# Kernel optimization log

Measured on AMD Instinct MI355X. Metric: run time of the kernel, lower is better.

Reference implementation:

```python
import jax, jax.numpy as jnp
import numpy as np

EMBED_DIM = 256
DEPTH = 4
N_EMBED = 8192
COMMIT_W = 0.25


def setup_inputs() -> dict:
    key = jax.random.key(0)
    kx, kc = jax.random.split(key)
    x = jax.random.normal(kx, (8, 1024, EMBED_DIM), dtype=jnp.float32)
    # stacked per-depth codebooks, last row is the padding row (unused by argmin path)
    codebooks = jax.random.normal(kc, (DEPTH, N_EMBED + 1, EMBED_DIM), dtype=jnp.float32) * 0.05
    return {"x": x, "codebooks": codebooks}


def _quantize_once(residual, cb):
    # residual: [..., D], cb: [K, D]
    D = cb.shape[-1]
    flat = residual.reshape(-1, D)                              # [N, D]
    dist = (jnp.sum(flat * flat, axis=1, keepdims=True)
            + jnp.sum(cb * cb, axis=1)[None, :]
            - 2.0 * (flat @ cb.T))                              # [N, K]
    idx = jnp.argmin(dist, axis=-1)                             # [N]
    quant = cb[idx].reshape(residual.shape)                     # gather
    return quant, idx.reshape(residual.shape[:-1])


def reference(x, codebooks):
    depth = codebooks.shape[0]
    residual = jax.lax.stop_gradient(x)
    agg = jnp.zeros_like(x)
    loss = jnp.float32(0.0)
    codes = []
    for d in range(depth):  # small fixed depth loop (structurally distinct codebooks)
        cb = jax.lax.stop_gradient(codebooks[d, :-1, :])        # drop padding row
        quant, idx = _quantize_once(residual, cb)
        residual = residual - quant
        agg = agg + quant                                       # partial-sum quant at depth d
        codes.append(idx)
        # commitment loss term: mse(x, partial_quant.detach())
        loss = loss + jnp.mean((x - jax.lax.stop_gradient(agg)) ** 2)
    commitment_loss = COMMIT_W * loss / depth
    # straight-through estimator
    out = x + jax.lax.stop_gradient(agg - x)
    code_idxs = jnp.stack(codes, axis=-1)                       # [..., depth]
    return out, commitment_loss, code_idxs
```

## Files before the change

kernel.cpp:

```cpp
#include <hip/hip_runtime.h>

#define NTOK   8192
#define DIM    256
#define NDEPTH 4
#define KROWS  8193
#define KARG   8192
#define NSLICE 8
#define FCAP   1024
#define EPSGAP 3e-3f

typedef __attribute__((ext_vector_type(8))) short short8v;
typedef __attribute__((ext_vector_type(4))) float float4v;

__device__ __forceinline__ unsigned short f2bf(float f) {
    unsigned int u = __float_as_uint(f);
    unsigned int r = (u + 0x7FFFu + ((u >> 16) & 1u)) >> 16;
    return (unsigned short)r;
}

__device__ __forceinline__ size_t fragIdx(int tile, int s, int lane, int e) {
    return ((((size_t)tile * 8 + s) * 64 + lane) * 8 + e);
}

__global__ void prep_tokens0(const float* __restrict__ x, unsigned short* __restrict__ rhB,
                             unsigned short* __restrict__ rlB, double* __restrict__ r64) {
    int t = blockIdx.x, i = threadIdx.x;
    float v = x[(size_t)t * DIM + i];
    r64[(size_t)t * DIM + i] = (double)v;
    unsigned short hb = f2bf(v);
    float hf = __uint_as_float(((unsigned int)hb) << 16);
    unsigned short lb = f2bf(v - hf);
    int T = t >> 4, n = t & 15;
    int s = i >> 5, kl = i & 31, g = kl >> 3, e = kl & 7;
    size_t idx = fragIdx(T, s, g * 16 + n, e);
    rhB[idx] = hb;
    rlB[idx] = lb;
}

__global__ void cnorm_kernel(const float* __restrict__ cbs, double* __restrict__ cnorm64,
                             float* __restrict__ cnorm32) {
    int d    = blockIdx.y;
    int row  = blockIdx.x * 4 + (threadIdx.x >> 6);
    int lane = threadIdx.x & 63;
    const float* c = cbs + ((size_t)d * KROWS + row) * DIM;
    float4 v = *(const float4*)(c + lane * 4);
    double s = (double)v.x * v.x + (double)v.y * v.y + (double)v.z * v.z + (double)v.w * v.w;
    #pragma unroll
    for (int o = 32; o > 0; o >>= 1) s += __shfl_down(s, o, 64);
    if (lane == 0) {
        cnorm64[(size_t)d * KARG + row] = s;
        cnorm32[(size_t)d * KARG + row] = (float)s;
    }
}

__global__ void prep_codes(const float* __restrict__ cbs, unsigned short* __restrict__ chA,
                           unsigned short* __restrict__ clA) {
    int bid = blockIdx.x;
    int d = bid >> 13, j = bid & 8191;
    int i = threadIdx.x;
    float v = cbs[((size_t)d * KROWS + j) * DIM + i];
    unsigned short hb = f2bf(v);
    float hf = __uint_as_float(((unsigned int)hb) << 16);
    unsigned short lb = f2bf(v - hf);
    int CT = j >> 4, m = j & 15;
    int s = i >> 5, kl = i & 31, g = kl >> 3, e = kl & 7;
    size_t base = (size_t)d * KARG * DIM;
    size_t idx = base + fragIdx(CT, s, g * 16 + m, e);
    chA[idx] = hb;
    clA[idx] = lb;
}

__global__ __launch_bounds__(512, 2) void argmin_mfma2(const unsigned short* __restrict__ chA_d,
                                                       const unsigned short* __restrict__ clA_d,
                                                       const unsigned short* __restrict__ rhB,
                                                       const unsigned short* __restrict__ rlB,
                                                       const float* __restrict__ cn32_d,
                                                       float* __restrict__ sM1, int* __restrict__ sJ1,
                                                       float* __restrict__ sM2) {
    __shared__ unsigned short lds[2][2][16384];
    const int tid  = threadIdx.x;
    const int wave = tid >> 6, lane = tid & 63;
    const int tg = blockIdx.x >> 3, slice = blockIdx.x & 7;
    const int g4 = lane >> 4, col = lane & 15;
    const float INF = __int_as_float(0x7f800000);

    const int T = tg * 8 + wave;
    short8v bh[8], bl[8];
    #pragma unroll
    for (int s = 0; s < 8; ++s) {
        bh[s] = *(const short8v*)(rhB + fragIdx(T, s, lane, 0));
        bl[s] = *(const short8v*)(rlB + fragIdx(T, s, lane, 0));
    }

    typedef const __attribute__((address_space(1))) unsigned int GUI;
    typedef __attribute__((address_space(3))) unsigned int LUI;
    auto stage = [&](int buf, int cg) {
        const unsigned short* gh = chA_d + ((size_t)(slice * 64 + cg * 4)) * 4096;
        const unsigned short* gl = clA_d + ((size_t)(slice * 64 + cg * 4)) * 4096;
        #pragma unroll
        for (int p = 0; p < 4; ++p) {
            int off = (p * 512 + tid) * 8;
            __builtin_amdgcn_global_load_lds((GUI*)(gh + off), (LUI*)(&lds[buf][0][off]), 16, 0, 0);
            __builtin_amdgcn_global_load_lds((GUI*)(gl + off), (LUI*)(&lds[buf][1][off]), 16, 0, 0);
        }
    };

    float M1 = INF, M2 = INF;
    int   J1 = 0;

    stage(0, 0);
    int buf = 0;
    for (int cg = 0; cg < 16; ++cg) {
        float4 cn[4];
        #pragma unroll
        for (int ct = 0; ct < 4; ++ct)
            cn[ct] = *(const float4*)(cn32_d + (slice * 64 + cg * 4 + ct) * 16 + g4 * 4);
        stage(buf ^ 1, cg + 1);
        asm volatile("s_waitcnt vmcnt(12)" ::: "memory");
        __builtin_amdgcn_s_barrier();

        float4v acc[4];
        #pragma unroll
        for (int ct = 0; ct < 4; ++ct) acc[ct] = (float4v){0.f, 0.f, 0.f, 0.f};
        #pragma unroll
        for (int s = 0; s < 8; ++s) {
            #pragma unroll
            for (int ct = 0; ct < 4; ++ct) {
                short8v ah = *(const short8v*)&lds[buf][0][((ct * 8 + s) * 64 + lane) * 8];
                short8v al = *(const short8v*)&lds[buf][1][((ct * 8 + s) * 64 + lane) * 8];
                acc[ct] = __builtin_amdgcn_mfma_f32_16x16x32_bf16(ah, bh[s], acc[ct], 0, 0, 0);
                acc[ct] = __builtin_amdgcn_mfma_f32_16x16x32_bf16(ah, bl[s], acc[ct], 0, 0, 0);
                acc[ct] = __builtin_amdgcn_mfma_f32_16x16x32_bf16(al, bh[s], acc[ct], 0, 0, 0);
            }
        }
        #pragma unroll
        for (int ct = 0; ct < 4; ++ct) {
            const int jb = (slice * 64 + cg * 4 + ct) * 16 + g4 * 4;
            float dv;
            dv = cn[ct].x - 2.0f * acc[ct][0];
            if (dv < M1) { M2 = M1; M1 = dv; J1 = jb + 0; } else if (dv < M2) M2 = dv;
            dv = cn[ct].y - 2.0f * acc[ct][1];
            if (dv < M1) { M2 = M1; M1 = dv; J1 = jb + 1; } else if (dv < M2) M2 = dv;
            dv = cn[ct].z - 2.0f * acc[ct][2];
            if (dv < M1) { M2 = M1; M1 = dv; J1 = jb + 2; } else if (dv < M2) M2 = dv;
            dv = cn[ct].w - 2.0f * acc[ct][3];
            if (dv < M1) { M2 = M1; M1 = dv; J1 = jb + 3; } else if (dv < M2) M2 = dv;
        }
        __builtin_amdgcn_s_barrier();
        buf ^= 1;
    }

    #pragma unroll
    for (int off = 16; off <= 32; off <<= 1) {
        float om1 = __shfl_xor(M1, off, 64);
        int   oj  = __shfl_xor(J1, off, 64);
        float om2 = __shfl_xor(M2, off, 64);
        if (om1 < M1 || (om1 == M1 && oj < J1)) {
            M2 = fminf(M1, om2); M1 = om1; J1 = oj;
        } else {
            M2 = fminf(M2, om1);
        }
    }
    if (g4 == 0) {
        int t = tg * 128 + wave * 16 + col;
        sM1[slice * NTOK + t] = M1;
        sJ1[slice * NTOK + t] = J1;
        sM2[slice * NTOK + t] = M2;
    }
}

__global__ void merge_flag8(const float* __restrict__ sM1, const int* __restrict__ sJ1,
                            const float* __restrict__ sM2, int* __restrict__ idxv,
                            int* __restrict__ flagList, int* __restrict__ flagCount) {
    int t = blockIdx.x * 256 + threadIdx.x;
    float m1 = sM1[t], m2 = sM2[t];
    int   j1 = sJ1[t];
    #pragma unroll
    for (int s = 1; s < NSLICE; ++s) {
        float a1 = sM1[s * NTOK + t], a2 = sM2[s * NTOK + t];
        int   aj = sJ1[s * NTOK + t];
        if (a1 < m1) { m2 = fminf(m1, a2); m1 = a1; j1 = aj; }
        else         { m2 = fminf(m2, a1); }
    }
    idxv[t] = j1;
    if (m2 - m1 <= EPSGAP) {
        int pos = atomicAdd(flagCount, 1);
        if (pos < FCAP) flagList[pos] = t;
    }
}

__global__ __launch_bounds__(256) void recheck_part(const double* __restrict__ rsrc,
                                                    const float* __restrict__ cb,
                                                    const double* __restrict__ cnorm,
                                                    const int* __restrict__ flagList,
                                                    const int* __restrict__ flagCount,
                                                    double* __restrict__ partD,
                                                    int* __restrict__ partJ) {
    const int slot = blockIdx.x >> 3;
    const int cnt  = min(*flagCount, FCAP);
    if (slot >= cnt) return;
    const int range = blockIdx.x & 7;
    const int tid   = threadIdx.x;
    const int tok   = flagList[slot];
    __shared__ double rs[DIM];
    __shared__ double sbest[256];
    __shared__ int    sbidx[256];
    rs[tid] = rsrc[(size_t)tok * DIM + tid];
    __syncthreads();

    double best = 1e300; int bestj = 0;
    for (int q = 0; q < 4; ++q) {
        const int j = range * 1024 + q * 256 + tid;
        const float* c = cb + (size_t)j * DIM;
        double acc = 0.0;
        #pragma unroll 1
        for (int i = 0; i < DIM; i += 4) {
            float4 cv = *(const float4*)(c + i);
            acc = fma((double)cv.w, rs[i + 3],
                  fma((double)cv.z, rs[i + 2],
                  fma((double)cv.y, rs[i + 1],
                  fma((double)cv.x, rs[i + 0], acc))));
        }
        double dist = cnorm[j] - 2.0 * acc;
        if (dist < best) { best = dist; bestj = j; }
    }
    sbest[tid] = best; sbidx[tid] = bestj;
    __syncthreads();
    for (int s = 128; s > 0; s >>= 1) {
        if (tid < s) {
            double ob = sbest[tid + s]; int oj = sbidx[tid + s];
            if (ob < sbest[tid] || (ob == sbest[tid] && oj < sbidx[tid])) {
                sbest[tid] = ob; sbidx[tid] = oj;
            }
        }
        __syncthreads();
    }
    if (tid == 0) { partD[slot * 8 + range] = sbest[0]; partJ[slot * 8 + range] = sbidx[0]; }
}

__global__ void recheck_merge(const int* __restrict__ flagList, const int* __restrict__ flagCount,
                              const double* __restrict__ partD, const int* __restrict__ partJ,
                              int* __restrict__ idxv) {
    int slot = blockIdx.x * 256 + threadIdx.x;
    int cnt  = min(*flagCount, FCAP);
    if (slot >= cnt) return;
    double best = partD[slot * 8]; int bestj = partJ[slot * 8];
    #pragma unroll
    for (int r = 1; r < 8; ++r) {
        double ob = partD[slot * 8 + r]; int oj = partJ[slot * 8 + r];
        if (ob < best) { best = ob; bestj = oj; }
    }
    idxv[flagList[slot]] = bestj;
}

__global__ void update_kernel(const float* __restrict__ x, const float* __restrict__ cb,
                              const int* __restrict__ idxv, double* __restrict__ resid,
                              float* __restrict__ out, double* __restrict__ lossSum,
                              float* __restrict__ codes_out, unsigned short* __restrict__ rhB,
                              unsigned short* __restrict__ rlB, int is_first) {
    const int t = blockIdx.x;
    const int i = threadIdx.x;
    const int idx = idxv[t];
    const size_t off = (size_t)t * DIM + i;
    float q = cb[(size_t)idx * DIM + i];
    double r_new = resid[off] - (double)q;
    resid[off] = r_new;
    float rv = (float)r_new;
    unsigned short hb = f2bf(rv);
    float hf = __uint_as_float(((unsigned int)hb) << 16);
    unsigned short lb = f2bf(rv - hf);
    {
        int T = t >> 4, n = t & 15;
        int s = i >> 5, kl = i & 31, g = kl >> 3, e = kl & 7;
        size_t fi = fragIdx(T, s, g * 16 + n, e);
        rhB[fi] = hb; rlB[fi] = lb;
    }
    float a_new = is_first ? q : (out[off] + q);
    out[off] = a_new;
    float diff = x[off] - a_new;
    double v = (double)diff * (double)diff;
    #pragma unroll
    for (int o = 32; o > 0; o >>= 1) v += __shfl_down(v, o, 64);
    __shared__ double wsum[4];
    int wid = i >> 6, lane = i & 63;
    if (lane == 0) wsum[wid] = v;
    __syncthreads();
    if (i == 0) {
        atomicAdd(lossSum, wsum[0] + wsum[1] + wsum[2] + wsum[3]);
        codes_out[(size_t)t * NDEPTH] = (float)idx;
    }
}

__global__ void final_kernel(float* __restrict__ out, const double* __restrict__ lossSum) {
    if (threadIdx.x == 0) {
        double s = (lossSum[0] + lossSum[1] + lossSum[2] + lossSum[3]) / (double)((size_t)NTOK * DIM);
        out[(size_t)NTOK * DIM] = (float)(0.25 * s / (double)NDEPTH);
    }
}

extern "C" void kernel_launch(void* const* d_in, const int* in_sizes, int n_in,
                              void* d_out, int out_size, void* d_ws, size_t ws_size,
                              hipStream_t stream) {
    const float* x   = (const float*)d_in[0];
    const float* cbs = (const float*)d_in[1];
    float* out = (float*)d_out;
    char* ws = (char*)d_ws;

    double*         resid64  = (double*)(ws);
    unsigned short* chA      = (unsigned short*)(ws + 16777216);
    unsigned short* clA      = (unsigned short*)(ws + 33554432);
    unsigned short* rhB      = (unsigned short*)(ws + 50331648);
    unsigned short* rlB      = (unsigned short*)(ws + 54525952);
    double*         cnorm64  = (double*)(ws + 58720256);
    float*          cnorm32  = (float*)(ws + 58982400);
    float*          sM1      = (float*)(ws + 59113472);
    int*            sJ1      = (int*)  (ws + 59375616);
    float*          sM2      = (float*)(ws + 59637760);
    int*            idxbuf   = (int*)  (ws + 59899904);
    int*            flagList = (int*)  (ws + 59932672);
    double*         partD    = (double*)(ws + 59936768);
    int*            partJ    = (int*)  (ws + 60002304);
    int*            flagCount= (int*)  (ws + 60035072);
    double*         lossSum  = (double*)(ws + 60035088);

    hipMemsetAsync(lossSum, 0, NDEPTH * sizeof(double), stream);
    prep_tokens0<<<NTOK, 256, 0, stream>>>(x, rhB, rlB, resid64);
    cnorm_kernel<<<dim3(KARG / 4, NDEPTH), 256, 0, stream>>>(cbs, cnorm64, cnorm32);
    prep_codes<<<NDEPTH * KARG, 256, 0, stream>>>(cbs, chA, clA);

    float* codes_base = out + (size_t)NTOK * DIM + 1;
    for (int d = 0; d < NDEPTH; ++d) {
        const float* cbd = cbs + (size_t)d * KROWS * DIM;
        hipMemsetAsync(flagCount, 0, sizeof(int), stream);
        argmin_mfma2<<<512, 512, 0, stream>>>(chA + (size_t)d * KARG * DIM,
                                              clA + (size_t)d * KARG * DIM,
                                              rhB, rlB, cnorm32 + (size_t)d * KARG,
                                              sM1, sJ1, sM2);
        merge_flag8<<<NTOK / 256, 256, 0, stream>>>(sM1, sJ1, sM2, idxbuf, flagList, flagCount);
        recheck_part<<<FCAP * 8, 256, 0, stream>>>(resid64, cbd, cnorm64 + (size_t)d * KARG,
                                                   flagList, flagCount, partD, partJ);
        recheck_merge<<<FCAP / 256, 256, 0, stream>>>(flagList, flagCount, partD, partJ, idxbuf);
        update_kernel<<<NTOK, 256, 0, stream>>>(x, cbd, idxbuf, resid64, out,
                                                lossSum + d, codes_base + d, rhB, rlB,
                                                d == 0 ? 1 : 0);
    }
    final_kernel<<<1, 64, 0, stream>>>(out, lossSum);
}
```

Measured before the change: 1.322 ms.

## Double token tiles per wave in argmin, fuse prep kernels and recheck merge

Each wave in the MFMA argmin kernel now processes two 16-token tiles instead of one, so every codebook fragment staged in LDS is reused across twice as many tokens and the grid is halved. The three preprocessing kernels are merged into one launch, with the code-norm reduction moved into the codebook-prep blocks. The recheck-merge kernel is folded into the update kernel through a per-token flag slot, and the per-depth memsets become one memset of per-depth counters. In exchange the argmin kernel holds more registers for B fragments and accumulators, and fewer blocks are launched.

Measured after the change: 1.217 ms. 7.9% less time.

```diff
diff --git a/kernel.cpp b/kernel.cpp
--- a/kernel.cpp
+++ b/kernel.cpp
@@ -22,55 +22,54 @@
     return ((((size_t)tile * 8 + s) * 64 + lane) * 8 + e);
 }
 
-__global__ void prep_tokens0(const float* __restrict__ x, unsigned short* __restrict__ rhB,
-                             unsigned short* __restrict__ rlB, double* __restrict__ r64) {
-    int t = blockIdx.x, i = threadIdx.x;
-    float v = x[(size_t)t * DIM + i];
-    r64[(size_t)t * DIM + i] = (double)v;
-    unsigned short hb = f2bf(v);
-    float hf = __uint_as_float(((unsigned int)hb) << 16);
-    unsigned short lb = f2bf(v - hf);
-    int T = t >> 4, n = t & 15;
-    int s = i >> 5, kl = i & 31, g = kl >> 3, e = kl & 7;
-    size_t idx = fragIdx(T, s, g * 16 + n, e);
-    rhB[idx] = hb;
-    rlB[idx] = lb;
-}
-
-__global__ void cnorm_kernel(const float* __restrict__ cbs, double* __restrict__ cnorm64,
-                             float* __restrict__ cnorm32) {
-    int d    = blockIdx.y;
-    int row  = blockIdx.x * 4 + (threadIdx.x >> 6);
-    int lane = threadIdx.x & 63;
-    const float* c = cbs + ((size_t)d * KROWS + row) * DIM;
-    float4 v = *(const float4*)(c + lane * 4);
-    double s = (double)v.x * v.x + (double)v.y * v.y + (double)v.z * v.z + (double)v.w * v.w;
-    #pragma unroll
-    for (int o = 32; o > 0; o >>= 1) s += __shfl_down(s, o, 64);
-    if (lane == 0) {
-        cnorm64[(size_t)d * KARG + row] = s;
-        cnorm32[(size_t)d * KARG + row] = (float)s;
-    }
-}
-
-__global__ void prep_codes(const float* __restrict__ cbs, unsigned short* __restrict__ chA,
-                           unsigned short* __restrict__ clA) {
-    int bid = blockIdx.x;
-    int d = bid >> 13, j = bid & 8191;
-    int i = threadIdx.x;
-    float v = cbs[((size_t)d * KROWS + j) * DIM + i];
-    unsigned short hb = f2bf(v);
-    float hf = __uint_as_float(((unsigned int)hb) << 16);
-    unsigned short lb = f2bf(v - hf);
-    int CT = j >> 4, m = j & 15;
-    int s = i >> 5, kl = i & 31, g = kl >> 3, e = kl & 7;
-    size_t base = (size_t)d * KARG * DIM;
-    size_t idx = base + fragIdx(CT, s, g * 16 + m, e);
-    chA[idx] = hb;
-    clA[idx] = lb;
-}
-
-__global__ __launch_bounds__(512, 2) void argmin_mfma2(const unsigned short* __restrict__ chA_d,
+__global__ void prep_all(const float* __restrict__ x, const float* __restrict__ cbs,
+                         unsigned short* __restrict__ rhB, unsigned short* __restrict__ rlB,
+                         double* __restrict__ r64, unsigned short* __restrict__ chA,
+                         unsigned short* __restrict__ clA, double* __restrict__ cnorm64,
+                         float* __restrict__ cnorm32) {
+    const int bid = blockIdx.x;
+    const int i = threadIdx.x;
+    if (bid < NTOK) {
+        int t = bid;
+        float v = x[(size_t)t * DIM + i];
+        r64[(size_t)t * DIM + i] = (double)v;
+        unsigned short hb = f2bf(v);
+        float hf = __uint_as_float(((unsigned int)hb) << 16);
+        unsigned short lb = f2bf(v - hf);
+        int T = t >> 4, n = t & 15;
+        int s = i >> 5, kl = i & 31, g = kl >> 3, e = kl & 7;
+        size_t idx = fragIdx(T, s, g * 16 + n, e);
+        rhB[idx] = hb;
+        rlB[idx] = lb;
+    } else {
+        int cid = bid - NTOK;
+        int d = cid >> 13, j = cid & 8191;
+        float v = cbs[((size_t)d * KROWS + j) * DIM + i];
+        unsigned short hb = f2bf(v);
+        float hf = __uint_as_float(((unsigned int)hb) << 16);
+        unsigned short lb = f2bf(v - hf);
+        int CT = j >> 4, m = j & 15;
+        int s = i >> 5, kl = i & 31, g = kl >> 3, e = kl & 7;
+        size_t base = (size_t)d * KARG * DIM;
+        size_t idx = base + fragIdx(CT, s, g * 16 + m, e);
+        chA[idx] = hb;
+        clA[idx] = lb;
+        double sq = (double)v * (double)v;
+        #pragma unroll
+        for (int o = 32; o > 0; o >>= 1) sq += __shfl_down(sq, o, 64);
+        __shared__ double wsum[4];
+        int wid = i >> 6, lane = i & 63;
+        if (lane == 0) wsum[wid] = sq;
+        __syncthreads();
+        if (i == 0) {
+            double sv = wsum[0] + wsum[1] + wsum[2] + wsum[3];
+            cnorm64[(size_t)d * KARG + j] = sv;
+            cnorm32[(size_t)d * KARG + j] = (float)sv;
+        }
+    }
+}
+
+__global__ __launch_bounds__(512, 2) void argmin_mfma3(const unsigned short* __restrict__ chA_d,
                                                        const unsigned short* __restrict__ clA_d,
                                                        const unsigned short* __restrict__ rhB,
                                                        const unsigned short* __restrict__ rlB,
@@ -84,12 +83,14 @@
     const int g4 = lane >> 4, col = lane & 15;
     const float INF = __int_as_float(0x7f800000);
 
-    const int T = tg * 8 + wave;
-    short8v bh[8], bl[8];
+    const int T0 = tg * 16 + wave * 2;
+    short8v bh0[8], bl0[8], bh1[8], bl1[8];
     #pragma unroll
     for (int s = 0; s < 8; ++s) {
-        bh[s] = *(const short8v*)(rhB + fragIdx(T, s, lane, 0));
-        bl[s] = *(const short8v*)(rlB + fragIdx(T, s, lane, 0));
+        bh0[s] = *(const short8v*)(rhB + fragIdx(T0,     s, lane, 0));
+        bl0[s] = *(const short8v*)(rlB + fragIdx(T0,     s, lane, 0));
+        bh1[s] = *(const short8v*)(rhB + fragIdx(T0 + 1, s, lane, 0));
+        bl1[s] = *(const short8v*)(rlB + fragIdx(T0 + 1, s, lane, 0));
     }
 
     typedef const __attribute__((address_space(1))) unsigned int GUI;
@@ -105,8 +106,8 @@
         }
     };
 
-    float M1 = INF, M2 = INF;
-    int   J1 = 0;
+    float M1[2] = {INF, INF}, M2[2] = {INF, INF};
+    int   J1[2] = {0, 0};
 
     stage(0, 0);
     int buf = 0;
@@ -119,32 +120,41 @@
         asm volatile("s_waitcnt vmcnt(12)" ::: "memory");
         __builtin_amdgcn_s_barrier();
 
-        float4v acc[4];
-        #pragma unroll
-        for (int ct = 0; ct < 4; ++ct) acc[ct] = (float4v){0.f, 0.f, 0.f, 0.f};
+        float4v acc[4][2];
+        #pragma unroll
+        for (int ct = 0; ct < 4; ++ct) {
+            acc[ct][0] = (float4v){0.f, 0.f, 0.f, 0.f};
+            acc[ct][1] = (float4v){0.f, 0.f, 0.f, 0.f};
+        }
         #pragma unroll
         for (int s = 0; s < 8; ++s) {
             #pragma unroll
             for (int ct = 0; ct < 4; ++ct) {
                 short8v ah = *(const short8v*)&lds[buf][0][((ct * 8 + s) * 64 + lane) * 8];
                 short8v al = *(const short8v*)&lds[buf][1][((ct * 8 + s) * 64 + lane) * 8];
-                acc[ct] = __builtin_amdgcn_mfma_f32_16x16x32_bf16(ah, bh[s], acc[ct], 0, 0, 0);
-                acc[ct] = __builtin_amdgcn_mfma_f32_16x16x32_bf16(ah, bl[s], acc[ct], 0, 0, 0);
-                acc[ct] = __builtin_amdgcn_mfma_f32_16x16x32_bf16(al, bh[s], acc[ct], 0, 0, 0);
+                acc[ct][0] = __builtin_amdgcn_mfma_f32_16x16x32_bf16(ah, bh0[s], acc[ct][0], 0, 0, 0);
+                acc[ct][0] = __builtin_amdgcn_mfma_f32_16x16x32_bf16(ah, bl0[s], acc[ct][0], 0, 0, 0);
+                acc[ct][0] = __builtin_amdgcn_mfma_f32_16x16x32_bf16(al, bh0[s], acc[ct][0], 0, 0, 0);
+                acc[ct][1] = __builtin_amdgcn_mfma_f32_16x16x32_bf16(ah, bh1[s], acc[ct][1], 0, 0, 0);
+                acc[ct][1] = __builtin_amdgcn_mfma_f32_16x16x32_bf16(ah, bl1[s], acc[ct][1], 0, 0, 0);
+                acc[ct][1] = __builtin_amdgcn_mfma_f32_16x16x32_bf16(al, bh1[s], acc[ct][1], 0, 0, 0);
             }
         }
         #pragma unroll
         for (int ct = 0; ct < 4; ++ct) {
             const int jb = (slice * 64 + cg * 4 + ct) * 16 + g4 * 4;
-            float dv;
-            dv = cn[ct].x - 2.0f * acc[ct][0];
-            if (dv < M1) { M2 = M1; M1 = dv; J1 = jb + 0; } else if (dv < M2) M2 = dv;
-            dv = cn[ct].y - 2.0f * acc[ct][1];
-            if (dv < M1) { M2 = M1; M1 = dv; J1 = jb + 1; } else if (dv < M2) M2 = dv;
-            dv = cn[ct].z - 2.0f * acc[ct][2];
-            if (dv < M1) { M2 = M1; M1 = dv; J1 = jb + 2; } else if (dv < M2) M2 = dv;
-            dv = cn[ct].w - 2.0f * acc[ct][3];
-            if (dv < M1) { M2 = M1; M1 = dv; J1 = jb + 3; } else if (dv < M2) M2 = dv;
+            #pragma unroll
+            for (int tt = 0; tt < 2; ++tt) {
+                float dv;
+                dv = cn[ct].x - 2.0f * acc[ct][tt][0];
+                if (dv < M1[tt]) { M2[tt] = M1[tt]; M1[tt] = dv; J1[tt] = jb + 0; } else if (dv < M2[tt]) M2[tt] = dv;
+                dv = cn[ct].y - 2.0f * acc[ct][tt][1];
+                if (dv < M1[tt]) { M2[tt] = M1[tt]; M1[tt] = dv; J1[tt] = jb + 1; } else if (dv < M2[tt]) M2[tt] = dv;
+                dv = cn[ct].z - 2.0f * acc[ct][tt][2];
+                if (dv < M1[tt]) { M2[tt] = M1[tt]; M1[tt] = dv; J1[tt] = jb + 2; } else if (dv < M2[tt]) M2[tt] = dv;
+                dv = cn[ct].w - 2.0f * acc[ct][tt][3];
+                if (dv < M1[tt]) { M2[tt] = M1[tt]; M1[tt] = dv; J1[tt] = jb + 3; } else if (dv < M2[tt]) M2[tt] = dv;
+            }
         }
         __builtin_amdgcn_s_barrier();
         buf ^= 1;
@@ -152,26 +162,33 @@
 
     #pragma unroll
     for (int off = 16; off <= 32; off <<= 1) {
-        float om1 = __shfl_xor(M1, off, 64);
-        int   oj  = __shfl_xor(J1, off, 64);
-        float om2 = __shfl_xor(M2, off, 64);
-        if (om1 < M1 || (om1 == M1 && oj < J1)) {
-            M2 = fminf(M1, om2); M1 = om1; J1 = oj;
-        } else {
-            M2 = fminf(M2, om1);
+        #pragma unroll
+        for (int tt = 0; tt < 2; ++tt) {
+            float om1 = __shfl_xor(M1[tt], off, 64);
+            int   oj  = __shfl_xor(J1[tt], off, 64);
+            float om2 = __shfl_xor(M2[tt], off, 64);
+            if (om1 < M1[tt] || (om1 == M1[tt] && oj < J1[tt])) {
+                M2[tt] = fminf(M1[tt], om2); M1[tt] = om1; J1[tt] = oj;
+            } else {
+                M2[tt] = fminf(M2[tt], om1);
+            }
         }
     }
     if (g4 == 0) {
-        int t = tg * 128 + wave * 16 + col;
-        sM1[slice * NTOK + t] = M1;
-        sJ1[slice * NTOK + t] = J1;
-        sM2[slice * NTOK + t] = M2;
+        #pragma unroll
+        for (int tt = 0; tt < 2; ++tt) {
+            int t = (T0 + tt) * 16 + col;
+            sM1[slice * NTOK + t] = M1[tt];
+            sJ1[slice * NTOK + t] = J1[tt];
+            sM2[slice * NTOK + t] = M2[tt];
+        }
     }
 }
 
 __global__ void merge_flag8(const float* __restrict__ sM1, const int* __restrict__ sJ1,
                             const float* __restrict__ sM2, int* __restrict__ idxv,
-                            int* __restrict__ flagList, int* __restrict__ flagCount) {
+                            int* __restrict__ flagList, int* __restrict__ flagCount,
+                            int* __restrict__ flagSlot) {
     int t = blockIdx.x * 256 + threadIdx.x;
     float m1 = sM1[t], m2 = sM2[t];
     int   j1 = sJ1[t];
@@ -183,10 +200,12 @@
         else         { m2 = fminf(m2, a1); }
     }
     idxv[t] = j1;
+    int slot = -1;
     if (m2 - m1 <= EPSGAP) {
-        int pos = atomicAdd(flagCount, 1);
-        if (pos < FCAP) flagList[pos] = t;
-    }
+        slot = atomicAdd(flagCount, 1);
+        if (slot < FCAP) flagList[slot] = t;
+    }
+    flagSlot[t] = slot;
 }
 
 __global__ __launch_bounds__(256) void recheck_part(const double* __restrict__ rsrc,
@@ -238,29 +257,26 @@
     if (tid == 0) { partD[slot * 8 + range] = sbest[0]; partJ[slot * 8 + range] = sbidx[0]; }
 }
 
-__global__ void recheck_merge(const int* __restrict__ flagList, const int* __restrict__ flagCount,
+__global__ void update_kernel(const float* __restrict__ x, const float* __restrict__ cb,
+                              const int* __restrict__ idxv, const int* __restrict__ flagSlot,
                               const double* __restrict__ partD, const int* __restrict__ partJ,
-                              int* __restrict__ idxv) {
-    int slot = blockIdx.x * 256 + threadIdx.x;
-    int cnt  = min(*flagCount, FCAP);
-    if (slot >= cnt) return;
-    double best = partD[slot * 8]; int bestj = partJ[slot * 8];
-    #pragma unroll
-    for (int r = 1; r < 8; ++r) {
-        double ob = partD[slot * 8 + r]; int oj = partJ[slot * 8 + r];
-        if (ob < best) { best = ob; bestj = oj; }
-    }
-    idxv[flagList[slot]] = bestj;
-}
-
-__global__ void update_kernel(const float* __restrict__ x, const float* __restrict__ cb,
-                              const int* __restrict__ idxv, double* __restrict__ resid,
-                              float* __restrict__ out, double* __restrict__ lossSum,
-                              float* __restrict__ codes_out, unsigned short* __restrict__ rhB,
-                              unsigned short* __restrict__ rlB, int is_first) {
+                              double* __restrict__ resid, float* __restrict__ out,
+                              double* __restrict__ lossSum, float* __restrict__ codes_out,
+                              unsigned short* __restrict__ rhB, unsigned short* __restrict__ rlB,
+                              int is_first) {
     const int t = blockIdx.x;
     const int i = threadIdx.x;
-    const int idx = idxv[t];
+    int idx = idxv[t];
+    const int slot = flagSlot[t];
+    if (slot >= 0 && slot < FCAP) {
+        double best = partD[slot * 8]; int bj = partJ[slot * 8];
+        #pragma unroll
+        for (int r = 1; r < 8; ++r) {
+            double ob = partD[slot * 8 + r]; int oj = partJ[slot * 8 + r];
+            if (ob < best) { best = ob; bj = oj; }
+        }
+        idx = bj;
+    }
     const size_t off = (size_t)t * DIM + i;
     float q = cb[(size_t)idx * DIM + i];
     double r_new = resid[off] - (double)q;
@@ -317,32 +333,31 @@
     int*            sJ1      = (int*)  (ws + 59375616);
     float*          sM2      = (float*)(ws + 59637760);
     int*            idxbuf   = (int*)  (ws + 59899904);
-    int*            flagList = (int*)  (ws + 59932672);
-    double*         partD    = (double*)(ws + 59936768);
-    int*            partJ    = (int*)  (ws + 60002304);
-    int*            flagCount= (int*)  (ws + 60035072);
-    double*         lossSum  = (double*)(ws + 60035088);
-
-    hipMemsetAsync(lossSum, 0, NDEPTH * sizeof(double), stream);
-    prep_tokens0<<<NTOK, 256, 0, stream>>>(x, rhB, rlB, resid64);
-    cnorm_kernel<<<dim3(KARG / 4, NDEPTH), 256, 0, stream>>>(cbs, cnorm64, cnorm32);
-    prep_codes<<<NDEPTH * KARG, 256, 0, stream>>>(cbs, chA, clA);
+    int*            flagSlot = (int*)  (ws + 59932672);
+    int*            flagList = (int*)  (ws + 59965440);
+    double*         partD    = (double*)(ws + 59969536);
+    int*            partJ    = (int*)  (ws + 60035072);
+    int*            flagCount= (int*)  (ws + 60067840);
+    double*         lossSum  = (double*)(ws + 60067856);
+
+    hipMemsetAsync(flagCount, 0, 48, stream);
+    prep_all<<<NTOK + NDEPTH * KARG, 256, 0, stream>>>(x, cbs, rhB, rlB, resid64,
+                                                       chA, clA, cnorm64, cnorm32);
 
     float* codes_base = out + (size_t)NTOK * DIM + 1;
     for (int d = 0; d < NDEPTH; ++d) {
         const float* cbd = cbs + (size_t)d * KROWS * DIM;
-        hipMemsetAsync(flagCount, 0, sizeof(int), stream);
-        argmin_mfma2<<<512, 512, 0, stream>>>(chA + (size_t)d * KARG * DIM,
+        argmin_mfma3<<<256, 512, 0, stream>>>(chA + (size_t)d * KARG * DIM,
                                               clA + (size_t)d * KARG * DIM,
                                               rhB, rlB, cnorm32 + (size_t)d * KARG,
                                               sM1, sJ1, sM2);
-        merge_flag8<<<NTOK / 256, 256, 0, stream>>>(sM1, sJ1, sM2, idxbuf, flagList, flagCount);
+        merge_flag8<<<NTOK / 256, 256, 0, stream>>>(sM1, sJ1, sM2, idxbuf,
+                                                    flagList, flagCount + d, flagSlot);
         recheck_part<<<FCAP * 8, 256, 0, stream>>>(resid64, cbd, cnorm64 + (size_t)d * KARG,
-                                                   flagList, flagCount, partD, partJ);
-        recheck_merge<<<FCAP / 256, 256, 0, stream>>>(flagList, flagCount, partD, partJ, idxbuf);
-        update_kernel<<<NTOK, 256, 0, stream>>>(x, cbd, idxbuf, resid64, out,
-                                                lossSum + d, codes_base + d, rhB, rlB,
-                                                d == 0 ? 1 : 0);
+                                                   flagList, flagCount + d, partD, partJ);
+        update_kernel<<<NTOK, 256, 0, stream>>>(x, cbd, idxbuf, flagSlot, partD, partJ,
+                                                resid64, out, lossSum + d, codes_base + d,
+                                                rhB, rlB, d == 0 ? 1 : 0);
     }
     final_kernel<<<1, 64, 0, stream>>>(out, lossSum);
 }
```
